# Kernel tuning notes

Hardware: AMD Instinct MI355X
Metric: run time of the kernel (lower is better)

## Reference

```python
import jax, jax.numpy as jnp
import numpy as np

EPS = 1e-5

def conv1x1_bn(x, W, b, gamma, beta, mean, var):
    # x: (B,C,H,W); W: (O,C) 1x1 conv; BN in eval mode with running stats
    y = jnp.einsum('bchw,oc->bohw', x, W) + b[None, :, None, None]
    scale = gamma / jnp.sqrt(var + EPS)
    return y * scale[None, :, None, None] + (beta - mean * scale)[None, :, None, None]

def setup_inputs() -> dict:
    key = jax.random.key(0)
    ks = jax.random.split(key, 12)
    B, C, H, W = 8, 64, 128, 256
    d = {
        'fea_left': jax.random.normal(ks[0], (B, C, H, W), jnp.float32),
        'fea_right': jax.random.normal(ks[1], (B, C, H, W), jnp.float32),
        'Wq': jax.random.normal(ks[2], (C, C), jnp.float32) * (1.0 / np.sqrt(C)),
        'bq': jax.random.normal(ks[3], (C,), jnp.float32) * 0.02,
        'gq': 1.0 + 0.1 * jax.random.normal(ks[4], (C,), jnp.float32),
        'betaq': 0.02 * jax.random.normal(ks[5], (C,), jnp.float32),
        'mq': 0.02 * jax.random.normal(ks[6], (C,), jnp.float32),
        'vq': jax.random.uniform(ks[7], (C,), jnp.float32, 0.5, 1.5),
        'Wk': jax.random.normal(ks[8], (C, C), jnp.float32) * (1.0 / np.sqrt(C)),
        'bk': jax.random.normal(ks[9], (C,), jnp.float32) * 0.02,
        'gk': 1.0 + 0.1 * jax.random.normal(ks[10], (C,), jnp.float32),
        'betak': 0.02 * jax.random.normal(ks[11], (C,), jnp.float32),
        'mk': 0.02 * jax.random.normal(jax.random.fold_in(key, 100), (C,), jnp.float32),
        'vk': jax.random.uniform(jax.random.fold_in(key, 101), (C,), jnp.float32, 0.5, 1.5),
    }
    return d

def _attend(src, tgt, Wq, bq, gq, betaq, mq, vq, Wk, bk, gk, betak, mk, vk):
    # query from src, key from tgt, values are raw tgt features
    c = src.shape[1]
    Q = conv1x1_bn(src, Wq, bq, gq, betaq, mq, vq)   # (B,C,H,W)
    K = conv1x1_bn(tgt, Wk, bk, gk, betak, mk, vk)   # (B,C,H,W)
    # cost: (B,H,Wq,Wk) = Q^T K over channels, per image row
    cost = jnp.einsum('bchw,bchv->bhwv', Q, K) / c
    attn = jax.nn.softmax(cost, axis=-1)
    out = jnp.einsum('bhwv,bchv->bchw', attn, tgt)   # back to (B,C,H,W)
    return out

def reference(fea_left, fea_right, Wq, bq, gq, betaq, mq, vq, Wk, bk, gk, betak, mk, vk):
    cxr = _attend(fea_left, fea_right, Wq, bq, gq, betaq, mq, vq, Wk, bk, gk, betak, mk, vk)
    enh = _attend(fea_right, fea_left, Wq, bq, gq, betaq, mq, vq, Wk, bk, gk, betak, mk, vk)
    return (cxr, enh)
```

## Files before the change

### kernel.cpp

```cpp
#include <hip/hip_runtime.h>
#include <hip/hip_bf16.h>

#define HW_ 32768
#define OUTHALF 16777216ULL
#define SMEM_BYTES 141312

typedef short short8  __attribute__((ext_vector_type(8)));
typedef short short4v __attribute__((ext_vector_type(4)));
typedef float f32x4   __attribute__((ext_vector_type(4)));
typedef unsigned int uint2v __attribute__((ext_vector_type(2)));
typedef unsigned int uint4v __attribute__((ext_vector_type(4)));

__device__ __forceinline__ unsigned short f2bf(float f) {
  unsigned u = __builtin_bit_cast(unsigned, f);
  u += 0x7fffu + ((u >> 16) & 1u);
  return (unsigned short)(u >> 16);
}
__device__ __forceinline__ short f2bfn(float f) {
  __hip_bfloat16 h = __float2bfloat16(f);
  return __builtin_bit_cast(short, h);
}
__device__ __forceinline__ unsigned pkw(float lo, float hi) {
  unsigned short a = (unsigned short)f2bfn(lo), b = (unsigned short)f2bfn(hi);
  return ((unsigned)b << 16) | (unsigned)a;
}
__device__ __forceinline__ char* swz(char* base, int row, int colByte) {
  return base + row * 128 + (colByte ^ ((row & 7) << 4));
}
__device__ __forceinline__ f32x4 zero4() { f32x4 z = {0.f, 0.f, 0.f, 0.f}; return z; }

__device__ __forceinline__ void xpose(const f32x4 (&p)[4], int g,
                                      short8& f0, short8& f1) {
  unsigned W00 = pkw(p[0][0], p[0][1]), W01 = pkw(p[0][2], p[0][3]);
  unsigned W10 = pkw(p[1][0], p[1][1]), W11 = pkw(p[1][2], p[1][3]);
  unsigned W20 = pkw(p[2][0], p[2][1]), W21 = pkw(p[2][2], p[2][3]);
  unsigned W30 = pkw(p[3][0], p[3][1]), W31 = pkw(p[3][2], p[3][3]);
  const bool h2 = (g & 2) != 0;
  unsigned SA0 = h2 ? W10 : W00, SA1 = h2 ? W11 : W01;
  unsigned SA2 = h2 ? W30 : W20, SA3 = h2 ? W31 : W21;
  unsigned SB0 = h2 ? W00 : W10, SB1 = h2 ? W01 : W11;
  unsigned SB2 = h2 ? W20 : W30, SB3 = h2 ? W21 : W31;
  unsigned ra0 = __shfl_xor((int)SA0, 16), ra1 = __shfl_xor((int)SA1, 16);
  unsigned ra2 = __shfl_xor((int)SA2, 16), ra3 = __shfl_xor((int)SA3, 16);
  unsigned rb0 = __shfl_xor((int)SB0, 32), rb1 = __shfl_xor((int)SB1, 32);
  unsigned rb2 = __shfl_xor((int)SB2, 32), rb3 = __shfl_xor((int)SB3, 32);
  unsigned rc0 = __shfl_xor((int)SB0, 48), rc1 = __shfl_xor((int)SB1, 48);
  unsigned rc2 = __shfl_xor((int)SB2, 48), rc3 = __shfl_xor((int)SB3, 48);
  unsigned a0 = g==0 ? SA0 : g==1 ? rc0 : g==2 ? rb0 : ra0;
  unsigned a1 = g==0 ? SA1 : g==1 ? rc1 : g==2 ? rb1 : ra1;
  unsigned a2 = g==0 ? SA2 : g==1 ? rc2 : g==2 ? rb2 : ra2;
  unsigned a3 = g==0 ? SA3 : g==1 ? rc3 : g==2 ? rb3 : ra3;
  unsigned b0 = g==3 ? SA0 : g==2 ? rc0 : g==1 ? rb0 : ra0;
  unsigned b1 = g==3 ? SA1 : g==2 ? rc1 : g==1 ? rb1 : ra1;
  unsigned b2 = g==3 ? SA2 : g==2 ? rc2 : g==1 ? rb2 : ra2;
  unsigned b3 = g==3 ? SA3 : g==2 ? rc3 : g==1 ? rb3 : ra3;
  uint4v u0 = {a0, a1, b0, b1};
  uint4v u1 = {a2, a3, b2, b3};
  f0 = __builtin_bit_cast(short8, u0);
  f1 = __builtin_bit_cast(short8, u1);
}

__global__ void pam_setup(const float* __restrict__ Wq, const float* __restrict__ bq,
                          const float* __restrict__ gq, const float* __restrict__ betaq,
                          const float* __restrict__ mq, const float* __restrict__ vq,
                          const float* __restrict__ Wk, const float* __restrict__ gk,
                          const float* __restrict__ vk,
                          short* __restrict__ Mbt, float* __restrict__ u) {
  int blk = blockIdx.x, tid = threadIdx.x;
  if (blk < 16) {
    int entry = blk * 256 + tid;
    int y = entry >> 6, x = entry & 63;
    float acc = 0.f;
    for (int o = 0; o < 64; ++o) {
      float sq = gq[o] * rsqrtf(vq[o] + 1e-5f);
      float sk = gk[o] * rsqrtf(vk[o] + 1e-5f);
      acc += Wq[o * 64 + x] * sq * Wk[o * 64 + y] * sk;
    }
    Mbt[y * 64 + x] = (short)f2bf(acc);
  } else if (tid < 64) {
    int y = tid;
    float acc = 0.f;
    for (int o = 0; o < 64; ++o) {
      float sq = gq[o] * rsqrtf(vq[o] + 1e-5f);
      float sk = gk[o] * rsqrtf(vk[o] + 1e-5f);
      float bqq = bq[o] * sq + betaq[o] - mq[o] * sq;
      acc += bqq * Wk[o * 64 + y] * sk;
    }
    u[y] = acc;
  }
}

__global__ __launch_bounds__(1024, 4) void pam_main(
    const float* __restrict__ fl, const float* __restrict__ fr,
    const short* __restrict__ Mbt, const float* __restrict__ uvec,
    float* __restrict__ out) {
  extern __shared__ __align__(16) char sm[];
  char* XLt = sm;
  char* XRt = sm + 32768;
  char* Xn  = sm + 65536;
  float* Db = (float*)(sm + 139264);

  const int tid  = threadIdx.x;
  const int lane = tid & 63;
  const int wave = tid >> 6;
  const int l15  = lane & 15;
  const int g    = lane >> 4;
  const int bb   = blockIdx.x >> 7;
  const int hh   = blockIdx.x & 127;
  const int rowOff = hh * 256;
  const int base_b = bb * 64;
  const int at   = wave >> 3;
  const int w0   = (wave & 7) * 32;

  #pragma unroll
  for (int it = 0; it < 2; ++it) {
    int u10 = (it * 1024 + tid) & 1023;
    int tensor = it;
    int cq = u10 & 15;
    int p  = ((u10 >> 4) & 63) * 4;
    const float* s = (tensor ? fr : fl) + (size_t)(base_b + cq * 4) * HW_ + rowOff + p;
    f32x4 a0 = *(const f32x4*)(s);
    f32x4 a1 = *(const f32x4*)(s + HW_);
    f32x4 a2 = *(const f32x4*)(s + 2 * HW_);
    f32x4 a3 = *(const f32x4*)(s + 3 * HW_);
    char* dst = tensor ? XRt : XLt;
    #pragma unroll
    for (int j = 0; j < 4; ++j) {
      short4v pk;
      pk[0] = f2bfn(a0[j]); pk[1] = f2bfn(a1[j]);
      pk[2] = f2bfn(a2[j]); pk[3] = f2bfn(a3[j]);
      *(short4v*)swz(dst, p + j, cq * 8) = pk;
    }
  }
  {
    const int dirT = tid >> 9;
    const int vcc  = (tid >> 3) & 63;
    const int vv8  = (tid & 7) * 8;
    const float* srcv = dirT ? fl : fr;
    const float* vbase = srcv + (size_t)(base_b + vcc) * HW_ + rowOff + vv8;
    char* XnW = Xn + dirT * 36864 + vcc * 144 + vv8 * 2;
    #pragma unroll
    for (int vt = 0; vt < 4; ++vt) {
      f32x4 A0 = *(const f32x4*)(vbase + vt * 64);
      f32x4 A1 = *(const f32x4*)(vbase + vt * 64 + 4);
      short8 pk;
      pk[0] = f2bfn(A0[0]); pk[1] = f2bfn(A0[1]);
      pk[2] = f2bfn(A0[2]); pk[3] = f2bfn(A0[3]);
      pk[4] = f2bfn(A1[0]); pk[5] = f2bfn(A1[1]);
      pk[6] = f2bfn(A1[2]); pk[7] = f2bfn(A1[3]);
      *(short8*)(XnW + vt * 9216) = pk;
    }
  }
  __syncthreads();

  char* Xq  = at ? XRt : XLt;
  char* Xkv = at ? XLt : XRt;
  char* XnC = Xn + at * 36864;

  short8 bq_[2][2];
  #pragma unroll
  for (int nj = 0; nj < 2; ++nj) {
    short8 xb0 = *(const short8*)swz(Xq, w0 + nj * 16 + l15, (8 * g) * 2);
    short8 xb1 = *(const short8*)swz(Xq, w0 + nj * 16 + l15, (32 + 8 * g) * 2);
    f32x4 qa[4];
    #pragma unroll
    for (int mi = 0; mi < 4; ++mi) {
      qa[mi] = zero4();
      short8 am0 = *(const short8*)(Mbt + (mi * 16 + l15) * 64 + 8 * g);
      short8 am1 = *(const short8*)(Mbt + (mi * 16 + l15) * 64 + 32 + 8 * g);
      qa[mi] = __builtin_amdgcn_mfma_f32_16x16x32_bf16(am0, xb0, qa[mi], 0, 0, 0);
      qa[mi] = __builtin_amdgcn_mfma_f32_16x16x32_bf16(am1, xb1, qa[mi], 0, 0, 0);
      f32x4 uv = *(const f32x4*)(uvec + mi * 16 + 4 * g);
      #pragma unroll
      for (int r = 0; r < 4; ++r)
        qa[mi][r] = (qa[mi][r] + uv[r]) * (0.015625f * 1.44269504089f);
    }
    xpose(qa, g, bq_[nj][0], bq_[nj][1]);
  }

  f32x4 acc_o[2][4];
  #pragma unroll
  for (int i = 0; i < 2; ++i)
    #pragma unroll
    for (int j = 0; j < 4; ++j) acc_o[i][j] = zero4();
  float dacc0 = 0.f, dacc1 = 0.f;

  #pragma unroll
  for (int vt = 0; vt < 4; ++vt) {
    f32x4 ps[2][4];
    #pragma unroll
    for (int mi = 0; mi < 4; ++mi) {
      short8 af0 = *(const short8*)swz(Xkv, vt * 64 + mi * 16 + l15, (8 * g) * 2);
      short8 af1 = *(const short8*)swz(Xkv, vt * 64 + mi * 16 + l15, (32 + 8 * g) * 2);
      #pragma unroll
      for (int nj = 0; nj < 2; ++nj) {
        ps[nj][mi] = zero4();
        ps[nj][mi] = __builtin_amdgcn_mfma_f32_16x16x32_bf16(af0, bq_[nj][0], ps[nj][mi], 0, 0, 0);
        ps[nj][mi] = __builtin_amdgcn_mfma_f32_16x16x32_bf16(af1, bq_[nj][1], ps[nj][mi], 0, 0, 0);
      }
    }
    #pragma unroll
    for (int nj = 0; nj < 2; ++nj) {
      float dl = 0.f;
      #pragma unroll
      for (int mi = 0; mi < 4; ++mi) {
        #pragma unroll
        for (int r = 0; r < 4; ++r)
          ps[nj][mi][r] = __builtin_amdgcn_exp2f(ps[nj][mi][r]);
        dl += ps[nj][mi][0] + ps[nj][mi][1] + ps[nj][mi][2] + ps[nj][mi][3];
      }
      if (nj == 0) dacc0 += dl; else dacc1 += dl;
    }
    char* XnT = XnC + vt * 9216;
    #pragma unroll
    for (int mi = 0; mi < 4; ++mi) {
      short4v bv[4];
      #pragma unroll
      for (int nj2 = 0; nj2 < 4; ++nj2)
        bv[nj2] = *(const short4v*)(XnT + (nj2 * 16 + l15) * 144 + (mi * 16 + 4 * g) * 2);
      #pragma unroll
      for (int nj = 0; nj < 2; ++nj) {
        uint2v pw;
        pw[0] = pkw(ps[nj][mi][0], ps[nj][mi][1]);
        pw[1] = pkw(ps[nj][mi][2], ps[nj][mi][3]);
        short4v pa = __builtin_bit_cast(short4v, pw);
        #pragma unroll
        for (int nj2 = 0; nj2 < 4; ++nj2)
          acc_o[nj][nj2] = __builtin_amdgcn_mfma_f32_16x16x16bf16_1k(
              pa, bv[nj2], acc_o[nj][nj2], 0, 0, 0);
      }
    }
  }

  float* outp = out + (at ? OUTHALF : 0) + (size_t)base_b * HW_ + rowOff;
  dacc0 += __shfl_xor(dacc0, 16); dacc0 += __shfl_xor(dacc0, 32);
  dacc1 += __shfl_xor(dacc1, 16); dacc1 += __shfl_xor(dacc1, 32);
  if (lane < 16) {
    Db[at * 256 + w0 + lane]      = __builtin_amdgcn_rcpf(dacc0);
    Db[at * 256 + w0 + 16 + lane] = __builtin_amdgcn_rcpf(dacc1);
  }
  #pragma unroll
  for (int nj = 0; nj < 2; ++nj) {
    f32x4 rd = *(const f32x4*)(Db + at * 256 + w0 + nj * 16 + 4 * g);
    #pragma unroll
    for (int nj2 = 0; nj2 < 4; ++nj2) {
      int c = nj2 * 16 + l15;
      f32x4 v;
      v[0] = acc_o[nj][nj2][0] * rd[0];
      v[1] = acc_o[nj][nj2][1] * rd[1];
      v[2] = acc_o[nj][nj2][2] * rd[2];
      v[3] = acc_o[nj][nj2][3] * rd[3];
      *(f32x4*)(outp + (size_t)c * HW_ + w0 + nj * 16 + 4 * g) = v;
    }
  }
}

extern "C" void kernel_launch(void* const* d_in, const int* in_sizes, int n_in,
                              void* d_out, int out_size, void* d_ws, size_t ws_size,
                              hipStream_t stream) {
  (void)in_sizes; (void)n_in; (void)out_size; (void)ws_size;
  const float* fl    = (const float*)d_in[0];
  const float* fr    = (const float*)d_in[1];
  const float* Wq    = (const float*)d_in[2];
  const float* bq    = (const float*)d_in[3];
  const float* gq    = (const float*)d_in[4];
  const float* betaq = (const float*)d_in[5];
  const float* mq    = (const float*)d_in[6];
  const float* vq    = (const float*)d_in[7];
  const float* Wk    = (const float*)d_in[8];
  const float* gk    = (const float*)d_in[10];
  const float* vk    = (const float*)d_in[13];
  short* Mbt = (short*)d_ws;
  float* u   = (float*)((char*)d_ws + 8192);
  float* out = (float*)d_out;

  hipFuncSetAttribute((const void*)pam_main,
                      hipFuncAttributeMaxDynamicSharedMemorySize, SMEM_BYTES);
  pam_setup<<<17, 256, 0, stream>>>(Wq, bq, gq, betaq, mq, vq, Wk, gk, vk, Mbt, u);
  pam_main<<<1024, 1024, SMEM_BYTES, stream>>>(fl, fr, Mbt, u, out);
}
```

Measured before the change: 112.1 us.

## Software-pipeline score MFMAs and compute softmax denominator via ones-vector MFMA

Restructures the attention inner loop so the QK score MFMAs for the next 16-key tile are issued before the exp and PV MFMAs of the current tile. The aim is to overlap matrix work with the transcendental and packing work and to shrink the live ps register array. The row-sum of exponentials is now taken with an extra MFMA against a ones column instead of scalar adds and cross-lane shuffles, using the bf16-rounded probabilities. This adds MFMA work and changes denominator rounding slightly.

```diff
diff --git a/kernel.cpp b/kernel.cpp
--- a/kernel.cpp
+++ b/kernel.cpp
@@ -183,62 +183,72 @@
   for (int i = 0; i < 2; ++i)
     #pragma unroll
     for (int j = 0; j < 4; ++j) acc_o[i][j] = zero4();
-  float dacc0 = 0.f, dacc1 = 0.f;
-
+  f32x4 acc_d[2];
+  acc_d[0] = zero4(); acc_d[1] = zero4();
+  short4v onesf;
+  {
+    short oz = (l15 == 0) ? (short)0x3F80 : (short)0;
+    onesf[0] = oz; onesf[1] = oz; onesf[2] = oz; onesf[3] = oz;
+  }
+
+  f32x4 psP[2], psN[2];
+  {
+    short8 a0 = *(const short8*)swz(Xkv, l15, (8 * g) * 2);
+    short8 a1 = *(const short8*)swz(Xkv, l15, (32 + 8 * g) * 2);
+    #pragma unroll
+    for (int nj = 0; nj < 2; ++nj) {
+      psP[nj] = __builtin_amdgcn_mfma_f32_16x16x32_bf16(a0, bq_[nj][0], zero4(), 0, 0, 0);
+      psP[nj] = __builtin_amdgcn_mfma_f32_16x16x32_bf16(a1, bq_[nj][1], psP[nj], 0, 0, 0);
+    }
+  }
   #pragma unroll
   for (int vt = 0; vt < 4; ++vt) {
-    f32x4 ps[2][4];
+    char* XnT = XnC + vt * 9216;
     #pragma unroll
     for (int mi = 0; mi < 4; ++mi) {
-      short8 af0 = *(const short8*)swz(Xkv, vt * 64 + mi * 16 + l15, (8 * g) * 2);
-      short8 af1 = *(const short8*)swz(Xkv, vt * 64 + mi * 16 + l15, (32 + 8 * g) * 2);
+      const int nvt = (mi < 3) ? vt : vt + 1;
+      const int nmi = (mi < 3) ? mi + 1 : 0;
+      if (nvt < 4) {
+        short8 a0 = *(const short8*)swz(Xkv, nvt * 64 + nmi * 16 + l15, (8 * g) * 2);
+        short8 a1 = *(const short8*)swz(Xkv, nvt * 64 + nmi * 16 + l15, (32 + 8 * g) * 2);
+        #pragma unroll
+        for (int nj = 0; nj < 2; ++nj) {
+          psN[nj] = __builtin_amdgcn_mfma_f32_16x16x32_bf16(a0, bq_[nj][0], zero4(), 0, 0, 0);
+          psN[nj] = __builtin_amdgcn_mfma_f32_16x16x32_bf16(a1, bq_[nj][1], psN[nj], 0, 0, 0);
+        }
+      }
+      short4v bv[4];
+      #pragma unroll
+      for (int nj2 = 0; nj2 < 4; ++nj2)
+        bv[nj2] = *(const short4v*)(XnT + (nj2 * 16 + l15) * 144 + (mi * 16 + 4 * g) * 2);
       #pragma unroll
       for (int nj = 0; nj < 2; ++nj) {
-        ps[nj][mi] = zero4();
-        ps[nj][mi] = __builtin_amdgcn_mfma_f32_16x16x32_bf16(af0, bq_[nj][0], ps[nj][mi], 0, 0, 0);
-        ps[nj][mi] = __builtin_amdgcn_mfma_f32_16x16x32_bf16(af1, bq_[nj][1], ps[nj][mi], 0, 0, 0);
-      }
-    }
-    #pragma unroll
-    for (int nj = 0; nj < 2; ++nj) {
-      float dl = 0.f;
-      #pragma unroll
-      for (int mi = 0; mi < 4; ++mi) {
+        f32x4 pv;
         #pragma unroll
         for (int r = 0; r < 4; ++r)
-          ps[nj][mi][r] = __builtin_amdgcn_exp2f(ps[nj][mi][r]);
-        dl += ps[nj][mi][0] + ps[nj][mi][1] + ps[nj][mi][2] + ps[nj][mi][3];
-      }
-      if (nj == 0) dacc0 += dl; else dacc1 += dl;
-    }
-    char* XnT = XnC + vt * 9216;
-    #pragma unroll
-    for (int mi = 0; mi < 4; ++mi) {
-      short4v bv[4];
-      #pragma unroll
-      for (int nj2 = 0; nj2 < 4; ++nj2)
-        bv[nj2] = *(const short4v*)(XnT + (nj2 * 16 + l15) * 144 + (mi * 16 + 4 * g) * 2);
-      #pragma unroll
-      for (int nj = 0; nj < 2; ++nj) {
+          pv[r] = __builtin_amdgcn_exp2f(psP[nj][r]);
         uint2v pw;
-        pw[0] = pkw(ps[nj][mi][0], ps[nj][mi][1]);
-        pw[1] = pkw(ps[nj][mi][2], ps[nj][mi][3]);
+        pw[0] = pkw(pv[0], pv[1]);
+        pw[1] = pkw(pv[2], pv[3]);
         short4v pa = __builtin_bit_cast(short4v, pw);
+        acc_d[nj] = __builtin_amdgcn_mfma_f32_16x16x16bf16_1k(pa, onesf, acc_d[nj], 0, 0, 0);
         #pragma unroll
         for (int nj2 = 0; nj2 < 4; ++nj2)
           acc_o[nj][nj2] = __builtin_amdgcn_mfma_f32_16x16x16bf16_1k(
               pa, bv[nj2], acc_o[nj][nj2], 0, 0, 0);
       }
-    }
-  }
-
+      psP[0] = psN[0]; psP[1] = psN[1];
+    }
+  }
+
+  if (l15 == 0) {
+    #pragma unroll
+    for (int nj = 0; nj < 2; ++nj)
+      #pragma unroll
+      for (int r = 0; r < 4; ++r)
+        Db[at * 256 + w0 + nj * 16 + 4 * g + r] = __builtin_amdgcn_rcpf(acc_d[nj][r]);
+  }
   float* outp = out + (at ? OUTHALF : 0) + (size_t)base_b * HW_ + rowOff;
-  dacc0 += __shfl_xor(dacc0, 16); dacc0 += __shfl_xor(dacc0, 32);
-  dacc1 += __shfl_xor(dacc1, 16); dacc1 += __shfl_xor(dacc1, 32);
-  if (lane < 16) {
-    Db[at * 256 + w0 + lane]      = __builtin_amdgcn_rcpf(dacc0);
-    Db[at * 256 + w0 + 16 + lane] = __builtin_amdgcn_rcpf(dacc1);
-  }
   #pragma unroll
   for (int nj = 0; nj < 2; ++nj) {
     f32x4 rd = *(const f32x4*)(Db + at * 256 + w0 + nj * 16 + 4 * g);
```

New measurement: 113.9 us. Within noise of the previous version (+1.7%).
